# Performance work log

Hardware: AMD Instinct MI355X
Metric: run time of the kernel (lower is better)

The kernel has to match this reference:

```python
import jax, jax.numpy as jnp
import numpy as np

B, S, D, F, UNITS = 32, 128, 32, 32, 11
NEG = -1.0e9


def setup_inputs() -> dict:
    key = jax.random.key(0)
    ks = jax.random.split(key, 8)
    X = jax.random.normal(ks[0], (B, S, D), dtype=jnp.float32)
    V = jax.random.normal(ks[1], (B, S, F), dtype=jnp.float32)
    # Dense(units) params (glorot-ish scale)
    sc = 1.0 / np.sqrt(D)
    W1 = jax.random.normal(ks[2], (D, UNITS), dtype=jnp.float32) * sc
    W2 = jax.random.normal(ks[3], (D, UNITS), dtype=jnp.float32) * sc
    W3 = jax.random.normal(ks[4], (D, UNITS), dtype=jnp.float32) * sc
    b1 = jnp.zeros((UNITS,), jnp.float32)
    b2 = jnp.zeros((UNITS,), jnp.float32)
    b3 = jnp.zeros((UNITS,), jnp.float32)
    return {"X": X, "V": V, "W1": W1, "b1": b1, "W2": W2, "b2": b2, "W3": W3, "b3": b3}


def reference(X, V, W1, b1, W2, b2, W3, b3):
    b, s, _ = X.shape
    # mask=None path: only the diagonal additive mask
    a = jnp.eye(s, dtype=X.dtype) * NEG  # [S,S]
    Q1 = X @ W1 + b1  # [B,S,U]
    Q2 = X @ W2 + b2
    Q3 = X @ W3 + b3
    A = jnp.einsum('biu,bju->bij', Q1, Q2) + a  # dot1 core
    Bm = jnp.einsum('bju,bku->bjk', Q2, Q3) + a  # dot2 core
    C = jnp.einsum('biu,bku->bik', Q1, Q3) + a  # dot3 core
    # threeway scores [B,S,S,S]
    scores = (A[:, :, :, None] + Bm[:, None, :, :] + C[:, :, None, :]) / 9.0
    # joint softmax over axes (1,2,3)
    p = jax.nn.softmax(scores.reshape(b, -1), axis=-1).reshape(b, s, s, s)
    # sum_{ijk} p_ijk * concat(V_i, V_j, V_k) = concat(m1@V, m2@V, m3@V)
    m1 = p.sum(axis=(2, 3))  # [B,S] marginal over i
    m2 = p.sum(axis=(1, 3))  # marginal over j
    m3 = p.sum(axis=(1, 2))  # marginal over k
    out1 = jnp.einsum('bs,bsf->bf', m1, V)
    out2 = jnp.einsum('bs,bsf->bf', m2, V)
    out3 = jnp.einsum('bs,bsf->bf', m3, V)
    return jnp.concatenate([out1, out2, out3], axis=-1)  # [B,3F]
```

## Files before the change

kernel.cpp:

```cpp
#include <hip/hip_runtime.h>
#include <hip/hip_bf16.h>


#define B_ 32
#define S_ 128
#define D_ 32
#define F_ 32
#define U_ 11
#define INV9 (1.0f / 9.0f)

__global__ __launch_bounds__(256) void k_qe(const float* __restrict__ X,
    const float* __restrict__ W1, const float* __restrict__ b1,
    const float* __restrict__ W2, const float* __restrict__ b2,
    const float* __restrict__ W3, const float* __restrict__ b3,
    float* __restrict__ E) {
    int blk = blockIdx.x;
    int b = blk & 31;
    int rest = blk >> 5;
    int m = rest >> 2;
    int tl = rest & 3;
    __shared__ float Wt[2][U_][32];
    __shared__ float bsh[2][U_];
    __shared__ float QRt[U_][S_];
    __shared__ float QLt[U_][32];
    int t = threadIdx.x;

    const float* WL = (m == 0) ? W1 : (m == 1) ? W2 : W1;
    const float* WR = (m == 0) ? W2 : (m == 1) ? W3 : W3;
    const float* bL = (m == 0) ? b1 : (m == 1) ? b2 : b1;
    const float* bR = (m == 0) ? b2 : (m == 1) ? b3 : b3;
    for (int idx = t; idx < 704; idx += 256) {
        int side = idx >= 352;
        int r = idx - side * 352;
        int u = r >> 5, d = r & 31;
        Wt[side][u][d] = (side ? WR : WL)[d * U_ + u];
    }
    if (t < 22) {
        int side = t >= U_;
        int u = side ? t - U_ : t;
        bsh[side][u] = (side ? bR : bL)[u];
    }
    __syncthreads();

    if (t < 160) {
        int isR = (t < 128);
        int row = isR ? t : (tl * 32 + (t - 128));
        const float* Xr = X + ((size_t)b * S_ + row) * D_;
        float4 xv[8];
#pragma unroll
        for (int q = 0; q < 8; ++q) xv[q] = ((const float4*)Xr)[q];
        float qv[U_];
#pragma unroll
        for (int u = 0; u < U_; ++u) qv[u] = bsh[isR][u];
#pragma unroll
        for (int d4 = 0; d4 < 8; ++d4) {
            float4 x = xv[d4];
#pragma unroll
            for (int u = 0; u < U_; ++u) {
                float4 w = *(const float4*)&Wt[isR][u][d4 * 4];
                qv[u] += x.x * w.x + x.y * w.y + x.z * w.z + x.w * w.w;
            }
        }
        if (isR) {
#pragma unroll
            for (int u = 0; u < U_; ++u) QRt[u][t] = qv[u];
        } else {
#pragma unroll
            for (int u = 0; u < U_; ++u) QLt[u][t - 128] = qv[u];
        }
    }
    __syncthreads();

    float* Eb = E + (size_t)(b * 3 + m) * (S_ * S_);
    int j4 = (t & 31) * 4;
    int il0 = (t >> 5) * 4;
    float4 qr[U_];
#pragma unroll
    for (int u = 0; u < U_; ++u) qr[u] = *(const float4*)&QRt[u][j4];
#pragma unroll
    for (int q = 0; q < 4; ++q) {
        int il = il0 + q;
        int i = tl * 32 + il;
        float s0 = 0, s1 = 0, s2 = 0, s3v = 0;
#pragma unroll
        for (int u = 0; u < U_; ++u) {
            float ql = QLt[u][il];
            s0 += ql * qr[u].x; s1 += ql * qr[u].y;
            s2 += ql * qr[u].z; s3v += ql * qr[u].w;
        }
        float4 e;
        e.x = (j4 + 0 == i) ? 0.f : __expf(s0 * INV9);
        e.y = (j4 + 1 == i) ? 0.f : __expf(s1 * INV9);
        e.z = (j4 + 2 == i) ? 0.f : __expf(s2 * INV9);
        e.w = (j4 + 3 == i) ? 0.f : __expf(s3v * INV9);
        *(float4*)&Eb[(size_t)i * S_ + j4] = e;
    }
}

__global__ __launch_bounds__(256, 4) void k_marg(const float* __restrict__ E,
    float* __restrict__ m1p, float* __restrict__ m2p, float* __restrict__ m3p) {
    int bid = blockIdx.x;
    int b   = bid & 31;
    int job = (bid >> 5) & 1;
    int cc  = (bid >> 6) & 7;
    int kh  = bid >> 9;
    int c0  = cc * 16, kk0 = kh * 64;
    const float* EA = E + (size_t)b * 3 * S_ * S_;
    const float* EB = EA + S_ * S_;
    const float* EC = EB + S_ * S_;
    const float* Bsrc = job ? EC : EB;
    const float* Wsrc = job ? EB : EC;

    __shared__ float At[16][132];
    __shared__ float Bs[16][68];
    float* red = &At[0][0];

    int t = threadIdx.x;

    if (job == 0) {
#pragma unroll
        for (int q = 0; q < 2; ++q) {
            int idx = t + q * 256;
            int i = idx >> 2;
            int j4 = (idx & 3) * 4;
            float4 v = *(const float4*)&EA[(size_t)i * S_ + c0 + j4];
            At[j4 + 0][i] = v.x; At[j4 + 1][i] = v.y;
            At[j4 + 2][i] = v.z; At[j4 + 3][i] = v.w;
        }
    } else {
#pragma unroll
        for (int q = 0; q < 2; ++q) {
            int idx = t + q * 256;
            int cl = idx >> 5;
            int col4 = (idx & 31) * 4;
            *(float4*)&At[cl][col4] =
                *(const float4*)&EA[(size_t)(c0 + cl) * S_ + col4];
        }
    }
    {
        int cl = t >> 4;
        int k4 = (t & 15) * 4;
        *(float4*)&Bs[cl][k4] =
            *(const float4*)&Bsrc[(size_t)(c0 + cl) * S_ + kk0 + k4];
    }
    __syncthreads();

    int r0 = (t >> 4) * 8;
    int k0 = (t & 15) * 4;
    float acc[8][4] = {};
#pragma unroll
    for (int c = 0; c < 16; ++c) {
        float4 a0 = *(const float4*)&At[c][r0];
        float4 a1 = *(const float4*)&At[c][r0 + 4];
        float4 bv = *(const float4*)&Bs[c][k0];
        float av[8] = {a0.x, a0.y, a0.z, a0.w, a1.x, a1.y, a1.z, a1.w};
#pragma unroll
        for (int x = 0; x < 8; ++x) {
            acc[x][0] += av[x] * bv.x; acc[x][1] += av[x] * bv.y;
            acc[x][2] += av[x] * bv.z; acc[x][3] += av[x] * bv.w;
        }
    }

    float rs[8], cs[4] = {0.f, 0.f, 0.f, 0.f};
#pragma unroll
    for (int x = 0; x < 8; ++x) {
        float4 w = *(const float4*)&Wsrc[(size_t)(r0 + x) * S_ + kk0 + k0];
        float v0 = w.x * acc[x][0], v1 = w.y * acc[x][1];
        float v2 = w.z * acc[x][2], v3 = w.w * acc[x][3];
        rs[x] = v0 + v1 + v2 + v3;
        cs[0] += v0; cs[1] += v1; cs[2] += v2; cs[3] += v3;
    }
#pragma unroll
    for (int x = 0; x < 8; ++x) {
        rs[x] += __shfl_xor(rs[x], 1);
        rs[x] += __shfl_xor(rs[x], 2);
        rs[x] += __shfl_xor(rs[x], 4);
        rs[x] += __shfl_xor(rs[x], 8);
    }
    if ((t & 15) == 0) {
        float* MO = job ? m2p : m1p;
        size_t base = ((size_t)b * 16 + cc * 2 + kh) * S_ + r0;
#pragma unroll
        for (int x = 0; x < 8; ++x) MO[base + x] = rs[x];
    }
    if (!job) {
#pragma unroll
        for (int y = 0; y < 4; ++y) {
            cs[y] += __shfl_xor(cs[y], 16);
            cs[y] += __shfl_xor(cs[y], 32);
        }
        __syncthreads();
        if ((t & 63) < 16) {
            int w = t >> 6;
            *(float4*)&red[w * 64 + k0] = make_float4(cs[0], cs[1], cs[2], cs[3]);
        }
        __syncthreads();
        if (t < 64)
            m3p[((size_t)b * 8 + cc) * S_ + kk0 + t] =
                red[t] + red[64 + t] + red[128 + t] + red[192 + t];
    }
}

__global__ __launch_bounds__(128) void k_out(const float* __restrict__ m1p,
    const float* __restrict__ m2p, const float* __restrict__ m3p,
    const float* __restrict__ V, float* __restrict__ out) {
    int b = blockIdx.x, t = threadIdx.x;
    __shared__ float ms[3][S_];
    __shared__ float Vs[S_][33];
    __shared__ float zr[2];
    const float* Vb = V + (size_t)b * S_ * F_;
#pragma unroll
    for (int q = 0; q < 8; ++q) {
        int idx = t + q * 128;
        int row = idx >> 3, c4 = (idx & 7) * 4;
        float4 v = *(const float4*)&Vb[row * F_ + c4];
        Vs[row][c4 + 0] = v.x; Vs[row][c4 + 1] = v.y;
        Vs[row][c4 + 2] = v.z; Vs[row][c4 + 3] = v.w;
    }
    size_t b16 = (size_t)b * 16 * S_ + t;
    float v1 = 0.f, v2 = 0.f;
#pragma unroll
    for (int p = 0; p < 16; ++p) {
        v1 += m1p[b16 + p * S_];
        v2 += m2p[b16 + p * S_];
    }
    size_t b8 = (size_t)b * 8 * S_ + t;
    float v3 = 0.f;
#pragma unroll
    for (int p = 0; p < 8; ++p) v3 += m3p[b8 + p * S_];
    ms[0][t] = v1; ms[1][t] = v2; ms[2][t] = v3;
    float z = v1;
#pragma unroll
    for (int off = 32; off; off >>= 1) z += __shfl_xor(z, off);
    if ((t & 63) == 0) zr[t >> 6] = z;
    __syncthreads();
    float invZ = 1.0f / (zr[0] + zr[1]);
    if (t < 96) {
        int which = t >> 5, f = t & 31;
        const float* ml = &ms[which][0];
        float s = 0.f;
#pragma unroll 8
        for (int s0 = 0; s0 < S_; ++s0) s += ml[s0] * Vs[s0][f];
        out[(size_t)b * 96 + t] = s * invZ;
    }
}

extern "C" void kernel_launch(void* const* d_in, const int* in_sizes, int n_in,
                              void* d_out, int out_size, void* d_ws, size_t ws_size,
                              hipStream_t stream) {
    const float* X  = (const float*)d_in[0];
    const float* V  = (const float*)d_in[1];
    const float* W1 = (const float*)d_in[2];
    const float* b1 = (const float*)d_in[3];
    const float* W2 = (const float*)d_in[4];
    const float* b2 = (const float*)d_in[5];
    const float* W3 = (const float*)d_in[6];
    const float* b3 = (const float*)d_in[7];
    float* out = (float*)d_out;

    float* E   = (float*)d_ws;
    float* m1p = E + (size_t)B_ * 3 * S_ * S_;
    float* m2p = m1p + (size_t)B_ * 16 * S_;
    float* m3p = m2p + (size_t)B_ * 16 * S_;

    k_qe<<<B_ * 12, 256, 0, stream>>>(X, W1, b1, W2, b2, W3, b3, E);
    k_marg<<<1024, 256, 0, stream>>>(E, m1p, m2p, m3p);
    k_out<<<B_, 128, 0, stream>>>(m1p, m2p, m3p, V, out);
}
```

Baseline: 19.89 us.

## Fuse output reduction into marginal kernel via last-block atomic counter

Removes the separate k_out launch. Each k_marg block publishes its partial marginals and increments a per-batch counter, and the last arriving block for a batch reduces the partials and computes the V-weighted output. The counter is reset in k_qe. This eliminates one kernel launch and its inter-kernel gap, at the cost of atomics, extra shared memory and tail work serialized on the last block.

New measurement: 33.71 us. 69.5% more time.

```diff
diff --git a/kernel.cpp b/kernel.cpp
--- a/kernel.cpp
+++ b/kernel.cpp
@@ -13,7 +13,7 @@
     const float* __restrict__ W1, const float* __restrict__ b1,
     const float* __restrict__ W2, const float* __restrict__ b2,
     const float* __restrict__ W3, const float* __restrict__ b3,
-    float* __restrict__ E) {
+    float* __restrict__ E, unsigned int* __restrict__ cnt) {
     int blk = blockIdx.x;
     int b = blk & 31;
     int rest = blk >> 5;
@@ -25,6 +25,8 @@
     __shared__ float QLt[U_][32];
     int t = threadIdx.x;
 
+    if (rest == 0 && t == 0) cnt[b] = 0u;
+
     const float* WL = (m == 0) ? W1 : (m == 1) ? W2 : W1;
     const float* WR = (m == 0) ? W2 : (m == 1) ? W3 : W3;
     const float* bL = (m == 0) ? b1 : (m == 1) ? b2 : b1;
@@ -98,7 +100,9 @@
 }
 
 __global__ __launch_bounds__(256, 4) void k_marg(const float* __restrict__ E,
-    float* __restrict__ m1p, float* __restrict__ m2p, float* __restrict__ m3p) {
+    float* __restrict__ m1p, float* __restrict__ m2p, float* __restrict__ m3p,
+    const float* __restrict__ V, float* __restrict__ out,
+    unsigned int* __restrict__ cnt) {
     int bid = blockIdx.x;
     int b   = bid & 31;
     int job = (bid >> 5) & 1;
@@ -111,9 +115,11 @@
     const float* Bsrc = job ? EC : EB;
     const float* Wsrc = job ? EB : EC;
 
-    __shared__ float At[16][132];
-    __shared__ float Bs[16][68];
-    float* red = &At[0][0];
+    __shared__ __align__(16) float pool[4624];
+    __shared__ int lastflag;
+    float* At = pool;
+    float* Bs = pool + 2112;
+    float* red = pool;
 
     int t = threadIdx.x;
 
@@ -121,11 +127,11 @@
 #pragma unroll
         for (int q = 0; q < 2; ++q) {
             int idx = t + q * 256;
-            int i = idx >> 2;
-            int j4 = (idx & 3) * 4;
-            float4 v = *(const float4*)&EA[(size_t)i * S_ + c0 + j4];
-            At[j4 + 0][i] = v.x; At[j4 + 1][i] = v.y;
-            At[j4 + 2][i] = v.z; At[j4 + 3][i] = v.w;
+            int i  = idx >> 2;
+            int jj = (idx & 3) * 4;
+            float4 v = *(const float4*)&EA[(size_t)i * S_ + c0 + jj];
+            At[(jj + 0) * 132 + i] = v.x; At[(jj + 1) * 132 + i] = v.y;
+            At[(jj + 2) * 132 + i] = v.z; At[(jj + 3) * 132 + i] = v.w;
         }
     } else {
 #pragma unroll
@@ -133,14 +139,14 @@
             int idx = t + q * 256;
             int cl = idx >> 5;
             int col4 = (idx & 31) * 4;
-            *(float4*)&At[cl][col4] =
+            *(float4*)&At[cl * 132 + col4] =
                 *(const float4*)&EA[(size_t)(c0 + cl) * S_ + col4];
         }
     }
     {
         int cl = t >> 4;
         int k4 = (t & 15) * 4;
-        *(float4*)&Bs[cl][k4] =
+        *(float4*)&Bs[cl * 68 + k4] =
             *(const float4*)&Bsrc[(size_t)(c0 + cl) * S_ + kk0 + k4];
     }
     __syncthreads();
@@ -150,9 +156,9 @@
     float acc[8][4] = {};
 #pragma unroll
     for (int c = 0; c < 16; ++c) {
-        float4 a0 = *(const float4*)&At[c][r0];
-        float4 a1 = *(const float4*)&At[c][r0 + 4];
-        float4 bv = *(const float4*)&Bs[c][k0];
+        float4 a0 = *(const float4*)&At[c * 132 + r0];
+        float4 a1 = *(const float4*)&At[c * 132 + r0 + 4];
+        float4 bv = *(const float4*)&Bs[c * 68 + k0];
         float av[8] = {a0.x, a0.y, a0.z, a0.w, a1.x, a1.y, a1.z, a1.w};
 #pragma unroll
         for (int x = 0; x < 8; ++x) {
@@ -181,7 +187,9 @@
         float* MO = job ? m2p : m1p;
         size_t base = ((size_t)b * 16 + cc * 2 + kh) * S_ + r0;
 #pragma unroll
-        for (int x = 0; x < 8; ++x) MO[base + x] = rs[x];
+        for (int x = 0; x < 8; ++x)
+            __hip_atomic_store(&MO[base + x], rs[x], __ATOMIC_RELAXED,
+                               __HIP_MEMORY_SCOPE_AGENT);
     }
     if (!job) {
 #pragma unroll
@@ -196,52 +204,63 @@
         }
         __syncthreads();
         if (t < 64)
-            m3p[((size_t)b * 8 + cc) * S_ + kk0 + t] =
-                red[t] + red[64 + t] + red[128 + t] + red[192 + t];
-    }
-}
-
-__global__ __launch_bounds__(128) void k_out(const float* __restrict__ m1p,
-    const float* __restrict__ m2p, const float* __restrict__ m3p,
-    const float* __restrict__ V, float* __restrict__ out) {
-    int b = blockIdx.x, t = threadIdx.x;
-    __shared__ float ms[3][S_];
-    __shared__ float Vs[S_][33];
-    __shared__ float zr[2];
-    const float* Vb = V + (size_t)b * S_ * F_;
-#pragma unroll
-    for (int q = 0; q < 8; ++q) {
-        int idx = t + q * 128;
-        int row = idx >> 3, c4 = (idx & 7) * 4;
-        float4 v = *(const float4*)&Vb[row * F_ + c4];
-        Vs[row][c4 + 0] = v.x; Vs[row][c4 + 1] = v.y;
-        Vs[row][c4 + 2] = v.z; Vs[row][c4 + 3] = v.w;
-    }
-    size_t b16 = (size_t)b * 16 * S_ + t;
-    float v1 = 0.f, v2 = 0.f;
-#pragma unroll
-    for (int p = 0; p < 16; ++p) {
-        v1 += m1p[b16 + p * S_];
-        v2 += m2p[b16 + p * S_];
-    }
-    size_t b8 = (size_t)b * 8 * S_ + t;
-    float v3 = 0.f;
-#pragma unroll
-    for (int p = 0; p < 8; ++p) v3 += m3p[b8 + p * S_];
-    ms[0][t] = v1; ms[1][t] = v2; ms[2][t] = v3;
-    float z = v1;
-#pragma unroll
-    for (int off = 32; off; off >>= 1) z += __shfl_xor(z, off);
-    if ((t & 63) == 0) zr[t >> 6] = z;
-    __syncthreads();
-    float invZ = 1.0f / (zr[0] + zr[1]);
-    if (t < 96) {
-        int which = t >> 5, f = t & 31;
-        const float* ml = &ms[which][0];
-        float s = 0.f;
+            __hip_atomic_store(&m3p[((size_t)b * 8 + cc) * S_ + kk0 + t],
+                               red[t] + red[64 + t] + red[128 + t] + red[192 + t],
+                               __ATOMIC_RELAXED, __HIP_MEMORY_SCOPE_AGENT);
+    }
+
+    asm volatile("s_waitcnt vmcnt(0)" ::: "memory");
+    __syncthreads();
+    if (t == 0)
+        lastflag = (__hip_atomic_fetch_add(&cnt[b], 1u, __ATOMIC_ACQ_REL,
+                                           __HIP_MEMORY_SCOPE_AGENT) == 31u) ? 1 : 0;
+    __syncthreads();
+
+    if (lastflag) {
+        float* Vs = pool;
+        float* ms = pool + 4224;
+        float* zr = pool + 4608;
+        const float* Vb = V + (size_t)b * S_ * F_;
+#pragma unroll
+        for (int q = 0; q < 4; ++q) {
+            int idx = t + q * 256;
+            int row = idx >> 3, c4 = (idx & 7) * 4;
+            float4 v = *(const float4*)&Vb[row * F_ + c4];
+            Vs[row * 33 + c4 + 0] = v.x; Vs[row * 33 + c4 + 1] = v.y;
+            Vs[row * 33 + c4 + 2] = v.z; Vs[row * 33 + c4 + 3] = v.w;
+        }
+        float v1 = 0.f;
+        if (t < S_) {
+            size_t b16 = (size_t)b * 16 * S_ + t;
+            float v2 = 0.f, v3 = 0.f;
+#pragma unroll
+            for (int p = 0; p < 16; ++p) {
+                v1 += __hip_atomic_load(&m1p[b16 + p * S_], __ATOMIC_RELAXED,
+                                        __HIP_MEMORY_SCOPE_AGENT);
+                v2 += __hip_atomic_load(&m2p[b16 + p * S_], __ATOMIC_RELAXED,
+                                        __HIP_MEMORY_SCOPE_AGENT);
+            }
+            size_t b8 = (size_t)b * 8 * S_ + t;
+#pragma unroll
+            for (int p = 0; p < 8; ++p)
+                v3 += __hip_atomic_load(&m3p[b8 + p * S_], __ATOMIC_RELAXED,
+                                        __HIP_MEMORY_SCOPE_AGENT);
+            ms[t] = v1; ms[S_ + t] = v2; ms[2 * S_ + t] = v3;
+        }
+        float z = v1;
+#pragma unroll
+        for (int off = 32; off; off >>= 1) z += __shfl_xor(z, off);
+        if ((t & 63) == 0) zr[t >> 6] = z;
+        __syncthreads();
+        float invZ = 1.0f / (zr[0] + zr[1] + zr[2] + zr[3]);
+        if (t < 96) {
+            int which = t >> 5, f = t & 31;
+            const float* ml = &ms[which * S_];
+            float s = 0.f;
 #pragma unroll 8
-        for (int s0 = 0; s0 < S_; ++s0) s += ml[s0] * Vs[s0][f];
-        out[(size_t)b * 96 + t] = s * invZ;
+            for (int s0 = 0; s0 < S_; ++s0) s += ml[s0] * Vs[s0 * 33 + f];
+            out[(size_t)b * 96 + t] = s * invZ;
+        }
     }
 }
 
@@ -262,8 +281,8 @@
     float* m1p = E + (size_t)B_ * 3 * S_ * S_;
     float* m2p = m1p + (size_t)B_ * 16 * S_;
     float* m3p = m2p + (size_t)B_ * 16 * S_;
-
-    k_qe<<<B_ * 12, 256, 0, stream>>>(X, W1, b1, W2, b2, W3, b3, E);
-    k_marg<<<1024, 256, 0, stream>>>(E, m1p, m2p, m3p);
-    k_out<<<B_, 128, 0, stream>>>(m1p, m2p, m3p, V, out);
+    unsigned int* cnt = (unsigned int*)(m3p + (size_t)B_ * 8 * S_);
+
+    k_qe<<<B_ * 12, 256, 0, stream>>>(X, W1, b1, W2, b2, W3, b3, E, cnt);
+    k_marg<<<1024, 256, 0, stream>>>(E, m1p, m2p, m3p, V, out, cnt);
 }
```
